# Optimization experiments

Measured on AMD Instinct MI355X. Metric: run time of the kernel, lower is better.

Reference implementation:

```python
import jax, jax.numpy as jnp
import numpy as np

HEADS = 4; C = 128; D = C // HEADS; L = 2
TKG_LEN = 24; NU = 2000; NL = 5000; E = 40000
B = 64; S = 128; MAX_USER = 5000; MAX_LOC = 10000


def _seg_softmax(logits, seg, num_seg):
    # per-destination-node softmax over incoming edges, per head. logits: [E, H]
    m = jax.ops.segment_max(logits, seg, num_segments=num_seg)
    e = jnp.exp(logits - m[seg])
    z = jax.ops.segment_sum(e, seg, num_segments=num_seg)
    return e / (z[seg] + 1e-16)


def _hgt_layer(xu, xl, src_ul, dst_ul, src_lu, dst_lu, wu, bu, wl, bl, ra, rm, rp, skip):
    # PyG HGTConv math. wu/wl: [4,C,C] (k,q,v,a), bu/bl: [4,C];
    # ra/rm: [2,H,D,D] per edge type (0: user->loc, 1: loc->user); rp: [2,H]; skip: [2] (user, loc)
    def kqv(x, w, b):
        return [(x @ w[i] + b[i]).reshape(-1, HEADS, D) for i in range(3)]
    ku, qu, vu = kqv(xu, wu, bu)
    kl, ql, vl = kqv(xl, wl, bl)
    scale = 1.0 / np.sqrt(D).astype(np.float32)

    def edge_msg(k_src, v_src, q_dst, src, dst, a_rel, m_rel, p_rel, n_dst):
        kr = jnp.einsum('nhd,hde->nhe', k_src, a_rel)   # relation-transformed keys
        mr = jnp.einsum('nhd,hde->nhe', v_src, m_rel)   # relation-transformed messages
        logits = (q_dst[dst] * kr[src]).sum(-1) * p_rel * scale  # [E, H]
        alpha = _seg_softmax(logits, dst, n_dst)
        return jax.ops.segment_sum(mr[src] * alpha[..., None], dst, num_segments=n_dst)  # [N,H,D]

    agg_l = edge_msg(ku, vu, ql, src_ul, dst_ul, ra[0], rm[0], rp[0], xl.shape[0])
    agg_u = edge_msg(kl, vl, qu, src_lu, dst_lu, ra[1], rm[1], rp[1], xu.shape[0])

    def update(agg, x, wa, ba, s):
        out = jax.nn.gelu(agg.reshape(-1, C), approximate=False) @ wa + ba
        g = jax.nn.sigmoid(s)
        return g * out + (1.0 - g) * x

    return (update(agg_u, xu, wu[3], bu[3], skip[0]),
            update(agg_l, xl, wl[3], bl[3], skip[1]))


def setup_inputs():
    key = jax.random.key(0)
    ks = jax.random.split(key, 20)
    w = lambda k, shape, s=0.05: jax.random.normal(k, shape, jnp.float32) * s
    user_emb = w(ks[0], (MAX_USER, C), 0.1).at[0].set(0.0)  # padding_idx=0
    loc_emb = w(ks[1], (MAX_LOC, C), 0.1).at[0].set(0.0)
    return dict(
        user_emb=user_emb, loc_emb=loc_emb,
        lin_user_w=w(ks[2], (C, C)), lin_user_b=jnp.zeros((C,), jnp.float32),
        lin_loc_w=w(ks[3], (C, C)), lin_loc_b=jnp.zeros((C,), jnp.float32),
        w_user=w(ks[4], (L, 4, C, C)), b_user=jnp.zeros((L, 4, C), jnp.float32),
        w_loc=w(ks[5], (L, 4, C, C)), b_loc=jnp.zeros((L, 4, C), jnp.float32),
        rel_a=w(ks[6], (L, 2, HEADS, D, D), 1.0 / np.sqrt(D)),
        rel_m=w(ks[7], (L, 2, HEADS, D, D), 1.0 / np.sqrt(D)),
        rel_p=jnp.ones((L, 2, HEADS), jnp.float32),
        skip=jnp.ones((L, 2), jnp.float32),
        lin2_w=w(ks[8], (C, C)), lin2_b=jnp.zeros((C,), jnp.float32),
        user_ids=jax.random.randint(ks[9], (TKG_LEN, NU), 0, MAX_USER),
        loc_ids=jax.random.randint(ks[10], (TKG_LEN, NL), 0, MAX_LOC),
        ei_ul_src=jax.random.randint(ks[11], (TKG_LEN, E), 0, NU),
        ei_ul_dst=jax.random.randint(ks[12], (TKG_LEN, E), 0, NL),
        ei_lu_src=jax.random.randint(ks[13], (TKG_LEN, E), 0, NL),
        ei_lu_dst=jax.random.randint(ks[14], (TKG_LEN, E), 0, NU),
        traj=jax.random.randint(ks[15], (B, S), 0, NL),
        tkg_idx=jax.random.randint(ks[16], (B, S), 0, TKG_LEN),
    )


def reference(user_emb, loc_emb, lin_user_w, lin_user_b, lin_loc_w, lin_loc_b,
              w_user, b_user, w_loc, b_loc, rel_a, rel_m, rel_p, skip,
              lin2_w, lin2_b, user_ids, loc_ids, ei_ul_src, ei_ul_dst,
              ei_lu_src, ei_lu_dst, traj, tkg_idx):
    def encode(uid, lid, sul, dul, slu, dlu):
        # EmbeddingLayer lookup + AggregationLayer: per-node-type Linear + relu, HGT convs, lin2 on locations
        xu = jax.nn.relu(user_emb[uid] @ lin_user_w + lin_user_b)
        xl = jax.nn.relu(loc_emb[lid] @ lin_loc_w + lin_loc_b)
        for i in range(L):
            xu, xl = _hgt_layer(xu, xl, sul, dul, slu, dlu,
                                w_user[i], b_user[i], w_loc[i], b_loc[i],
                                rel_a[i], rel_m[i], rel_p[i], skip[i])
        return xl @ lin2_w + lin2_b

    # the torch loop over tkg_dl snapshots -> vmap over the tkg_len axis
    tkg_out = jax.vmap(encode)(user_ids, loc_ids, ei_ul_src, ei_ul_dst, ei_lu_src, ei_lu_dst)
    # tkg_filter: one-hot mask multiply-sum == direct gather tkg_out[tkg_idx[b,s], traj[b,s]]
    tkg_traj = tkg_out[tkg_idx, traj]  # [B, S, C]
    return (tkg_traj, tkg_out)
```

## Files before the change

### kernel.cpp

```cpp
#include <hip/hip_runtime.h>
#include <math.h>

#define T_LEN 24
#define NUU 2000
#define NLL 5000
#define NE 40000
#define CH 128
#define NH 4
#define HD 32
#define TCHUNK 8

typedef __attribute__((ext_vector_type(8))) short short8;
typedef __attribute__((ext_vector_type(4))) float f32x4;

static inline int cdiv(int a, int b) { return (a + b - 1) / b; }

__device__ __forceinline__ unsigned short f2bf(float x) {
    unsigned u = __float_as_uint(x);
    unsigned r = (u + 0x7fff + ((u >> 16) & 1)) >> 16;
    return (unsigned short)r;
}
__device__ __forceinline__ float bf2f(unsigned short h) {
    return __uint_as_float(((unsigned)h) << 16);
}
__device__ __forceinline__ float2 bf2x(unsigned u) {
    float2 r;
    r.x = __uint_as_float(u << 16);
    r.y = __uint_as_float(u & 0xffff0000u);
    return r;
}

__global__ void fill_zero_int(int* __restrict__ p, int n) {
    int i = blockIdx.x * blockDim.x + threadIdx.x;
    if (i < n) p[i] = 0;
}

__global__ void histo_kernel(const int* __restrict__ dst, int* __restrict__ deg, int n) {
    int idx = blockIdx.x * blockDim.x + threadIdx.x;
    if (idx >= T_LEN * NE) return;
    int t = idx / NE;
    atomicAdd(&deg[t * n + dst[idx]], 1);
}

__global__ __launch_bounds__(256) void scan_off(const int* __restrict__ deg, int* __restrict__ offo,
                                                int* __restrict__ cur, int n) {
    __shared__ int part[256];
    int t = blockIdx.x, tid = threadIdx.x;
    int items = (n + 255) / 256;
    int start = tid * items, end = min(start + items, n);
    const int* dt = deg + t * n;
    int s = 0;
    for (int i = start; i < end; ++i) s += dt[i];
    part[tid] = s;
    __syncthreads();
    for (int d = 1; d < 256; d <<= 1) {
        int v = (tid >= d) ? part[tid - d] : 0;
        __syncthreads();
        part[tid] += v;
        __syncthreads();
    }
    int run = part[tid] - s;
    int* ot = offo + t * (n + 1);
    int* ct = cur + t * n;
    if (tid == 0) ot[0] = 0;
    for (int i = start; i < end; ++i) {
        ct[i] = run;
        run += dt[i];
        ot[i + 1] = run;
    }
}

__global__ void scatter_src(const int* __restrict__ dst, const int* __restrict__ src,
                            int* __restrict__ cur, int* __restrict__ ssrc, int n) {
    int idx = blockIdx.x * blockDim.x + threadIdx.x;
    if (idx >= T_LEN * NE) return;
    int t = idx / NE;
    int d = dst[idx];
    int pos = atomicAdd(&cur[t * n + d], 1);
    ssrc[(size_t)t * NE + pos] = src[idx];
}

__global__ __launch_bounds__(256) void build_fused(
    const float* __restrict__ w, const float* __restrict__ b,
    const float* __restrict__ ra, const float* __restrict__ rm,
    float* __restrict__ Wf, float* __restrict__ bf) {
    int idx = blockIdx.x * 256 + threadIdx.x;
    if (idx >= 128 * 384) return;
    int c = idx / 384, col = idx - c * 384;
    if (col < 128) {
        Wf[c * 384 + col] = w[16384 + c * 128 + col];
        if (c == 0) bf[col] = b[128 + col];
    } else {
        int sec = (col - 128) >> 7;
        int hc = (col - 128) & 127;
        int h = hc >> 5, e2 = hc & 31;
        const float* A = (sec == 0 ? ra : rm) + h * 1024;
        const float* wsrc = w + (sec == 0 ? 0 : 2) * 16384;
        const float* bsrc = b + (sec == 0 ? 0 : 2) * 128;
        float s = 0.f, sb = 0.f;
#pragma unroll
        for (int d = 0; d < 32; ++d) {
            float a = A[d * 32 + e2];
            s += wsrc[c * 128 + h * 32 + d] * a;
            sb += bsrc[h * 32 + d] * a;
        }
        Wf[c * 384 + col] = s;
        if (c == 0) bf[col] = sb;
    }
}

__global__ void bprep_kernel(const float* __restrict__ W, unsigned short* __restrict__ prep, int N) {
    int idx = blockIdx.x * blockDim.x + threadIdx.x;
    if (idx >= 128 * N) return;
    int k = idx / N, n = idx - k * N;
    float v = W[idx];
    unsigned short hi = f2bf(v);
    unsigned short lo = f2bf(v - bf2f(hi));
    int nt = n >> 6, nl = n & 63;
    size_t base = (size_t)nt * 16384 + (size_t)nl * 128 + k;
    prep[base] = hi;
    prep[base + 8192] = lo;
}

template <bool GATHER, int EPI>
__global__ __launch_bounds__(256) void gemm_mfma(
    const float* __restrict__ A, const int* __restrict__ ids,
    const unsigned short* __restrict__ prep, const float* __restrict__ bias,
    float* __restrict__ C, const float* __restrict__ Xold,
    const float* __restrict__ skipPtr, unsigned short* __restrict__ km,
    int M, int NC) {
    __shared__ __align__(16) char smem[65536];

    const int tid = threadIdx.x;
    const int lane = tid & 63;
    const int wid_w = tid >> 6;
    const int wm = wid_w >> 1, wn = wid_w & 1;
    const int l15 = lane & 15, l4 = lane >> 4;

    const int nx = gridDim.x, ny = gridDim.y;
    int flat = blockIdx.y * nx + blockIdx.x;
    int nwg = nx * ny;
    int q = nwg >> 3, r = nwg & 7;
    int xcd = flat & 7, rank = flat >> 3;
    int wgid = (xcd < r ? xcd * (q + 1) : r * (q + 1) + (xcd - r) * q) + rank;
    const int m0 = (wgid / ny) * 128;
    const int n0 = (wgid % ny) * 64;

    const unsigned short* bp = prep + (size_t)(wgid % ny) * 16384;
    short8 bh[2][4], bl[2][4];
#pragma unroll
    for (int nf = 0; nf < 2; ++nf) {
        int ncol = wn * 32 + nf * 16 + l15;
#pragma unroll
        for (int ks = 0; ks < 4; ++ks) {
            size_t off = (size_t)ncol * 128 + ks * 32 + l4 * 8;
            bh[nf][ks] = *(const short8*)(bp + off);
            bl[nf][ks] = *(const short8*)(bp + 8192 + off);
        }
    }

#pragma unroll
    for (int i = 0; i < 16; ++i) {
        int flat2 = i * 256 + tid;
        int rr = flat2 >> 5, c4 = flat2 & 31;
        int gr = m0 + rr;
        if (gr >= M) gr = M - 1;
        int arow = GATHER ? ids[gr] : gr;
        float4 v = *(const float4*)(A + (size_t)arow * 128 + c4 * 4);
        unsigned short h0 = f2bf(v.x), h1 = f2bf(v.y), h2 = f2bf(v.z), h3 = f2bf(v.w);
        unsigned short q0 = f2bf(v.x - bf2f(h0)), q1 = f2bf(v.y - bf2f(h1));
        unsigned short q2 = f2bf(v.z - bf2f(h2)), q3 = f2bf(v.w - bf2f(h3));
        uint2 hp, lp;
        hp.x = (unsigned)h0 | ((unsigned)h1 << 16);
        hp.y = (unsigned)h2 | ((unsigned)h3 << 16);
        lp.x = (unsigned)q0 | ((unsigned)q1 << 16);
        lp.y = (unsigned)q2 | ((unsigned)q3 << 16);
        int off = rr * 256 + ((c4 * 8) ^ ((rr & 7) << 4));
        *(uint2*)(smem + off) = hp;
        *(uint2*)(smem + 32768 + off) = lp;
    }
    __syncthreads();

    f32x4 acc[4][2];
#pragma unroll
    for (int m = 0; m < 4; ++m)
#pragma unroll
        for (int nf = 0; nf < 2; ++nf) acc[m][nf] = (f32x4)0.f;

#pragma unroll
    for (int ks = 0; ks < 4; ++ks) {
        short8 ah[4], al[4];
#pragma unroll
        for (int m = 0; m < 4; ++m) {
            int row = wm * 64 + m * 16 + l15;
            int off = row * 256 + ((ks * 64 + l4 * 16) ^ ((row & 7) << 4));
            ah[m] = *(const short8*)(smem + off);
            al[m] = *(const short8*)(smem + 32768 + off);
        }
#pragma unroll
        for (int m = 0; m < 4; ++m)
#pragma unroll
            for (int nf = 0; nf < 2; ++nf) {
                acc[m][nf] = __builtin_amdgcn_mfma_f32_16x16x32_bf16(al[m], bh[nf][ks], acc[m][nf], 0, 0, 0);
                acc[m][nf] = __builtin_amdgcn_mfma_f32_16x16x32_bf16(ah[m], bl[nf][ks], acc[m][nf], 0, 0, 0);
                acc[m][nf] = __builtin_amdgcn_mfma_f32_16x16x32_bf16(ah[m], bh[nf][ks], acc[m][nf], 0, 0, 0);
            }
    }

    float g = 0.f;
    if (EPI == 2) g = 1.f / (1.f + expf(-skipPtr[0]));
    float bias_v[2];
#pragma unroll
    for (int nf = 0; nf < 2; ++nf) bias_v[nf] = bias[n0 + wn * 32 + nf * 16 + l15];

#pragma unroll
    for (int m = 0; m < 4; ++m) {
#pragma unroll
        for (int nf = 0; nf < 2; ++nf) {
            int gc = n0 + wn * 32 + nf * 16 + l15;
#pragma unroll
            for (int i = 0; i < 4; ++i) {
                int gr = m0 + wm * 64 + m * 16 + l4 * 4 + i;
                if (gr >= M) continue;
                float x = acc[m][nf][i] + bias_v[nf];
                if (EPI == 1) x = fmaxf(x, 0.f);
                if (EPI == 2) {
                    float xo = Xold[(size_t)gr * NC + gc];
                    x = g * x + (1.f - g) * xo;
                }
                if (EPI == 3) {
                    if (gc < 128) C[(size_t)gr * 128 + gc] = x;
                    else km[(size_t)gr * 256 + (gc - 128)] = f2bf(x);
                } else {
                    C[(size_t)gr * NC + gc] = x;
                }
            }
        }
    }
}

__global__ __launch_bounds__(256) void agg_edges(
    const float* __restrict__ qD,
    const unsigned short* __restrict__ kmS,
    const int* __restrict__ off,
    const int* __restrict__ ssrc,
    const float* __restrict__ relp,
    float* __restrict__ agg,
    int nDst, int nSrc, int tBase) {
    int idx = blockIdx.x * 256 + threadIdx.x;
    int total = TCHUNK * nDst * NH * 8;
    if (idx >= total) return;
    int h = idx & 3;
    int slot = (idx >> 2) & 7;
    int node = (idx >> 5) % nDst;
    int tl = (idx >> 5) / nDst;
    int t = tBase + tl;

    size_t drow = (size_t)(tl * nDst + node);
    float p = relp[h] * 0.17677669529663687f;

    const float4* qp = (const float4*)(qD + drow * 128 + h * HD);
    float qr[HD];
#pragma unroll
    for (int j = 0; j < 8; j++) {
        float4 v = qp[j];
        qr[4 * j + 0] = v.x * p; qr[4 * j + 1] = v.y * p;
        qr[4 * j + 2] = v.z * p; qr[4 * j + 3] = v.w * p;
    }

    float m = -INFINITY, z = 0.f;
    float acc[HD];
#pragma unroll
    for (int d = 0; d < HD; d++) acc[d] = 0.f;

    int e0 = off[t * (nDst + 1) + node], e1 = off[t * (nDst + 1) + node + 1];
    const int* ssT = ssrc + (size_t)t * NE;

    for (int i = e0 + slot; i < e1; i += 8) {
        int s = ssT[i];
        const uint4* kp = (const uint4*)(kmS + ((size_t)(tl * nSrc + s)) * 256);
        uint ku[16], mu_[16];
        *(uint4*)(ku + 0) = kp[h * 4 + 0];
        *(uint4*)(ku + 4) = kp[h * 4 + 1];
        *(uint4*)(ku + 8) = kp[h * 4 + 2];
        *(uint4*)(ku + 12) = kp[h * 4 + 3];
        *(uint4*)(mu_ + 0) = kp[16 + h * 4 + 0];
        *(uint4*)(mu_ + 4) = kp[16 + h * 4 + 1];
        *(uint4*)(mu_ + 8) = kp[16 + h * 4 + 2];
        *(uint4*)(mu_ + 12) = kp[16 + h * 4 + 3];

        float dot = 0.f;
#pragma unroll
        for (int j = 0; j < 16; ++j) {
            float2 f = bf2x(ku[j]);
            dot = fmaf(qr[2 * j], f.x, dot);
            dot = fmaf(qr[2 * j + 1], f.y, dot);
        }
        float mn = fmaxf(m, dot);
        float c = __expf(m - mn);
        float w = __expf(dot - mn);
        z = z * c + w;
#pragma unroll
        for (int j = 0; j < 16; ++j) {
            float2 f = bf2x(mu_[j]);
            acc[2 * j] = fmaf(w, f.x, acc[2 * j] * c);
            acc[2 * j + 1] = fmaf(w, f.y, acc[2 * j + 1] * c);
        }
        m = mn;
    }

#pragma unroll
    for (int lm = 4; lm <= 16; lm <<= 1) {
        float mo = __shfl_xor(m, lm);
        float zo = __shfl_xor(z, lm);
        float mn = fmaxf(m, mo);
        float s1 = (m > -INFINITY) ? __expf(m - mn) : 0.f;
        float s2 = (mo > -INFINITY) ? __expf(mo - mn) : 0.f;
        z = z * s1 + zo * s2;
#pragma unroll
        for (int d = 0; d < HD; d++) {
            float ao = __shfl_xor(acc[d], lm);
            acc[d] = acc[d] * s1 + ao * s2;
        }
        m = mn;
    }

    if (slot == 0) {
        float inv = 1.f / (z + 1e-16f);
        float* op = agg + drow * CH + h * HD;
#pragma unroll
        for (int d = 0; d < HD; d++) {
            float v = acc[d] * inv;
            v = 0.5f * v * (1.f + erff(v * 0.70710678118654752f));
            op[d] = v;
        }
    }
}

__global__ void gather_traj(const float* __restrict__ tkg, const int* __restrict__ traj,
                            const int* __restrict__ tki, float* __restrict__ outp) {
    int idx = blockIdx.x * blockDim.x + threadIdx.x;
    if (idx >= 64 * 128 * 128) return;
    int r = idx >> 7, c2 = idx & 127;
    int t = tki[r], n = traj[r];
    outp[idx] = tkg[((size_t)t * NLL + n) * CH + c2];
}

extern "C" void kernel_launch(void* const* d_in, const int* in_sizes, int n_in,
                              void* d_out, int out_size, void* d_ws, size_t ws_size,
                              hipStream_t stream) {
    (void)in_sizes; (void)n_in; (void)out_size; (void)ws_size;
    const float* user_emb = (const float*)d_in[0];
    const float* loc_emb = (const float*)d_in[1];
    const float* lin_user_w = (const float*)d_in[2];
    const float* lin_user_b = (const float*)d_in[3];
    const float* lin_loc_w = (const float*)d_in[4];
    const float* lin_loc_b = (const float*)d_in[5];
    const float* w_user = (const float*)d_in[6];
    const float* b_user = (const float*)d_in[7];
    const float* w_loc = (const float*)d_in[8];
    const float* b_loc = (const float*)d_in[9];
    const float* rel_a = (const float*)d_in[10];
    const float* rel_m = (const float*)d_in[11];
    const float* rel_p = (const float*)d_in[12];
    const float* skip = (const float*)d_in[13];
    const float* lin2_w = (const float*)d_in[14];
    const float* lin2_b = (const float*)d_in[15];
    const int* user_ids = (const int*)d_in[16];
    const int* loc_ids = (const int*)d_in[17];
    const int* ei_ul_src = (const int*)d_in[18];
    const int* ei_ul_dst = (const int*)d_in[19];
    const int* ei_lu_src = (const int*)d_in[20];
    const int* ei_lu_dst = (const int*)d_in[21];
    const int* traj = (const int*)d_in[22];
    const int* tkg_idx = (const int*)d_in[23];
    float* outp = (float*)d_out;

    size_t woff = 0;
    char* base = (char*)d_ws;
    auto carve = [&](size_t bytes) -> void* {
        void* p = base + woff;
        woff += (bytes + 255) & ~(size_t)255;
        return p;
    };
    float* xu = (float*)carve((size_t)T_LEN * NUU * 128 * 4);
    float* xl = (float*)carve((size_t)T_LEN * NLL * 128 * 4);
    float* q_u = (float*)carve((size_t)TCHUNK * NUU * 128 * 4);
    float* q_l = (float*)carve((size_t)TCHUNK * NLL * 128 * 4);
    unsigned short* km_u = (unsigned short*)carve((size_t)TCHUNK * NUU * 256 * 2);
    unsigned short* km_l = (unsigned short*)carve((size_t)TCHUNK * NLL * 256 * 2);
    float* agg_u = (float*)carve((size_t)TCHUNK * NUU * 128 * 4);
    float* agg_l = (float*)carve((size_t)TCHUNK * NLL * 128 * 4);
    float* wf_u = (float*)carve(128 * 384 * 4);
    float* bf_u = (float*)carve(384 * 4);
    float* wf_l = (float*)carve(128 * 384 * 4);
    float* bf_l = (float*)carve(384 * 4);
    int* deg_ul = (int*)carve((size_t)T_LEN * NLL * 4);
    int* cur_ul = (int*)carve((size_t)T_LEN * NLL * 4);
    int* off_ul = (int*)carve((size_t)T_LEN * (NLL + 1) * 4);
    int* ss_ul = (int*)carve((size_t)T_LEN * NE * 4);
    int* deg_lu = (int*)carve((size_t)T_LEN * NUU * 4);
    int* cur_lu = (int*)carve((size_t)T_LEN * NUU * 4);
    int* off_lu = (int*)carve((size_t)T_LEN * (NUU + 1) * 4);
    int* ss_lu = (int*)carve((size_t)T_LEN * NE * 4);
    unsigned short* bp_lin_u = (unsigned short*)carve(128 * 512);
    unsigned short* bp_lin_l = (unsigned short*)carve(128 * 512);
    unsigned short* bp_lin2 = (unsigned short*)carve(128 * 512);
    unsigned short* bp_upd_u[2] = {(unsigned short*)carve(128 * 512), (unsigned short*)carve(128 * 512)};
    unsigned short* bp_upd_l[2] = {(unsigned short*)carve(128 * 512), (unsigned short*)carve(128 * 512)};
    unsigned short* bp_wf_u = (unsigned short*)carve(384 * 512);
    unsigned short* bp_wf_l = (unsigned short*)carve(384 * 512);

    fill_zero_int<<<cdiv(T_LEN * NLL, 256), 256, 0, stream>>>(deg_ul, T_LEN * NLL);
    fill_zero_int<<<cdiv(T_LEN * NUU, 256), 256, 0, stream>>>(deg_lu, T_LEN * NUU);
    histo_kernel<<<cdiv(T_LEN * NE, 256), 256, 0, stream>>>(ei_ul_dst, deg_ul, NLL);
    histo_kernel<<<cdiv(T_LEN * NE, 256), 256, 0, stream>>>(ei_lu_dst, deg_lu, NUU);
    scan_off<<<T_LEN, 256, 0, stream>>>(deg_ul, off_ul, cur_ul, NLL);
    scan_off<<<T_LEN, 256, 0, stream>>>(deg_lu, off_lu, cur_lu, NUU);
    scatter_src<<<cdiv(T_LEN * NE, 256), 256, 0, stream>>>(ei_ul_dst, ei_ul_src, cur_ul, ss_ul, NLL);
    scatter_src<<<cdiv(T_LEN * NE, 256), 256, 0, stream>>>(ei_lu_dst, ei_lu_src, cur_lu, ss_lu, NUU);

    bprep_kernel<<<64, 256, 0, stream>>>(lin_user_w, bp_lin_u, 128);
    bprep_kernel<<<64, 256, 0, stream>>>(lin_loc_w, bp_lin_l, 128);
    bprep_kernel<<<64, 256, 0, stream>>>(lin2_w, bp_lin2, 128);
    for (int l = 0; l < 2; ++l) {
        bprep_kernel<<<64, 256, 0, stream>>>(w_user + (size_t)(l * 4 + 3) * 16384, bp_upd_u[l], 128);
        bprep_kernel<<<64, 256, 0, stream>>>(w_loc + (size_t)(l * 4 + 3) * 16384, bp_upd_l[l], 128);
    }

    gemm_mfma<true, 1><<<dim3(cdiv(T_LEN * NUU, 128), 2), 256, 0, stream>>>(
        user_emb, user_ids, bp_lin_u, lin_user_b, xu, nullptr, nullptr, nullptr, T_LEN * NUU, 128);
    gemm_mfma<true, 1><<<dim3(cdiv(T_LEN * NLL, 128), 2), 256, 0, stream>>>(
        loc_emb, loc_ids, bp_lin_l, lin_loc_b, xl, nullptr, nullptr, nullptr, T_LEN * NLL, 128);

    for (int l = 0; l < 2; ++l) {
        build_fused<<<cdiv(128 * 384, 256), 256, 0, stream>>>(
            w_user + (size_t)l * 4 * 16384, b_user + l * 512,
            rel_a + (size_t)(l * 2 + 0) * 4096, rel_m + (size_t)(l * 2 + 0) * 4096, wf_u, bf_u);
        build_fused<<<cdiv(128 * 384, 256), 256, 0, stream>>>(
            w_loc + (size_t)l * 4 * 16384, b_loc + l * 512,
            rel_a + (size_t)(l * 2 + 1) * 4096, rel_m + (size_t)(l * 2 + 1) * 4096, wf_l, bf_l);
        bprep_kernel<<<192, 256, 0, stream>>>(wf_u, bp_wf_u, 384);
        bprep_kernel<<<192, 256, 0, stream>>>(wf_l, bp_wf_l, 384);

        for (int tb = 0; tb < T_LEN; tb += TCHUNK) {
            const int MU = TCHUNK * NUU;
            const int ML = TCHUNK * NLL;
            float* xu_c = xu + (size_t)tb * NUU * 128;
            float* xl_c = xl + (size_t)tb * NLL * 128;

            gemm_mfma<false, 3><<<dim3(cdiv(MU, 128), 6), 256, 0, stream>>>(
                xu_c, nullptr, bp_wf_u, bf_u, q_u, nullptr, nullptr, km_u, MU, 384);
            gemm_mfma<false, 3><<<dim3(cdiv(ML, 128), 6), 256, 0, stream>>>(
                xl_c, nullptr, bp_wf_l, bf_l, q_l, nullptr, nullptr, km_l, ML, 384);

            agg_edges<<<cdiv(TCHUNK * NLL * NH * 8, 256), 256, 0, stream>>>(
                q_l, km_u, off_ul, ss_ul, rel_p + (l * 2 + 0) * 4, agg_l, NLL, NUU, tb);
            agg_edges<<<cdiv(TCHUNK * NUU * NH * 8, 256), 256, 0, stream>>>(
                q_u, km_l, off_lu, ss_lu, rel_p + (l * 2 + 1) * 4, agg_u, NUU, NLL, tb);

            gemm_mfma<false, 2><<<dim3(cdiv(MU, 128), 2), 256, 0, stream>>>(
                agg_u, nullptr, bp_upd_u[l], b_user + l * 512 + 384,
                xu_c, xu_c, skip + l * 2 + 0, nullptr, MU, 128);
            gemm_mfma<false, 2><<<dim3(cdiv(ML, 128), 2), 256, 0, stream>>>(
                agg_l, nullptr, bp_upd_l[l], b_loc + l * 512 + 384,
                xl_c, xl_c, skip + l * 2 + 1, nullptr, ML, 128);
        }
    }

    float* tkg_out = outp + (size_t)64 * 128 * 128;
    gemm_mfma<false, 0><<<dim3(cdiv(T_LEN * NLL, 128), 2), 256, 0, stream>>>(
        xl, nullptr, bp_lin2, lin2_b, tkg_out, nullptr, nullptr, nullptr, T_LEN * NLL, 128);

    gather_traj<<<cdiv(64 * 128 * 128, 256), 256, 0, stream>>>(tkg_out, traj, tkg_idx, outp);
}
```

Before: 1.659 ms.

## Merge edge-aggregation launches and halve per-node slots with two-edge unrolling

The two per-relation edge attention/aggregation kernels become a single launch that dispatches on block index. Each destination node/head now uses 4 lanes instead of 8. Each lane processes two edges per iteration, issuing both edges' key/message loads together and folding them into a single online-softmax update. This cuts the number of shuffle-reduction steps and launch overhead and raises memory-level parallelism per thread. The costs are higher register pressure and fewer threads in flight. Low-degree nodes may also be less balanced across lanes.

Result: faster. 1.546 ms (-6.8%).

```diff
diff --git a/kernel.cpp b/kernel.cpp
--- a/kernel.cpp
+++ b/kernel.cpp
@@ -239,21 +239,15 @@
     }
 }
 
-__global__ __launch_bounds__(256) void agg_edges(
-    const float* __restrict__ qD,
-    const unsigned short* __restrict__ kmS,
-    const int* __restrict__ off,
-    const int* __restrict__ ssrc,
-    const float* __restrict__ relp,
-    float* __restrict__ agg,
+__device__ __forceinline__ void agg_core(
+    int idx, const float* __restrict__ qD, const unsigned short* __restrict__ kmS,
+    const int* __restrict__ off, const int* __restrict__ ssrc,
+    const float* __restrict__ relp, float* __restrict__ agg,
     int nDst, int nSrc, int tBase) {
-    int idx = blockIdx.x * 256 + threadIdx.x;
-    int total = TCHUNK * nDst * NH * 8;
-    if (idx >= total) return;
     int h = idx & 3;
-    int slot = (idx >> 2) & 7;
-    int node = (idx >> 5) % nDst;
-    int tl = (idx >> 5) / nDst;
+    int slot = (idx >> 2) & 3;
+    int node = (idx >> 4) % nDst;
+    int tl = (idx >> 4) / nDst;
     int t = tBase + tl;
 
     size_t drow = (size_t)(tl * nDst + node);
@@ -276,7 +270,47 @@
     int e0 = off[t * (nDst + 1) + node], e1 = off[t * (nDst + 1) + node + 1];
     const int* ssT = ssrc + (size_t)t * NE;
 
-    for (int i = e0 + slot; i < e1; i += 8) {
+    int i = e0 + slot;
+    for (; i + 4 < e1; i += 8) {
+        int s0 = ssT[i], s1 = ssT[i + 4];
+        const uint4* kp0 = (const uint4*)(kmS + ((size_t)(tl * nSrc + s0)) * 256);
+        const uint4* kp1 = (const uint4*)(kmS + ((size_t)(tl * nSrc + s1)) * 256);
+        uint4 k0a = kp0[h * 4 + 0], k0b = kp0[h * 4 + 1], k0c = kp0[h * 4 + 2], k0d = kp0[h * 4 + 3];
+        uint4 m0a = kp0[16 + h * 4 + 0], m0b = kp0[16 + h * 4 + 1], m0c = kp0[16 + h * 4 + 2], m0d = kp0[16 + h * 4 + 3];
+        uint4 k1a = kp1[h * 4 + 0], k1b = kp1[h * 4 + 1], k1c = kp1[h * 4 + 2], k1d = kp1[h * 4 + 3];
+        uint4 m1a = kp1[16 + h * 4 + 0], m1b = kp1[16 + h * 4 + 1], m1c = kp1[16 + h * 4 + 2], m1d = kp1[16 + h * 4 + 3];
+
+        uint ku0[16], ku1[16], mu0[16], mu1[16];
+        *(uint4*)(ku0 + 0) = k0a; *(uint4*)(ku0 + 4) = k0b; *(uint4*)(ku0 + 8) = k0c; *(uint4*)(ku0 + 12) = k0d;
+        *(uint4*)(mu0 + 0) = m0a; *(uint4*)(mu0 + 4) = m0b; *(uint4*)(mu0 + 8) = m0c; *(uint4*)(mu0 + 12) = m0d;
+        *(uint4*)(ku1 + 0) = k1a; *(uint4*)(ku1 + 4) = k1b; *(uint4*)(ku1 + 8) = k1c; *(uint4*)(ku1 + 12) = k1d;
+        *(uint4*)(mu1 + 0) = m1a; *(uint4*)(mu1 + 4) = m1b; *(uint4*)(mu1 + 8) = m1c; *(uint4*)(mu1 + 12) = m1d;
+
+        float dot0 = 0.f, dot1 = 0.f;
+#pragma unroll
+        for (int j = 0; j < 16; ++j) {
+            float2 f0 = bf2x(ku0[j]);
+            float2 f1 = bf2x(ku1[j]);
+            dot0 = fmaf(qr[2 * j], f0.x, dot0);
+            dot0 = fmaf(qr[2 * j + 1], f0.y, dot0);
+            dot1 = fmaf(qr[2 * j], f1.x, dot1);
+            dot1 = fmaf(qr[2 * j + 1], f1.y, dot1);
+        }
+        float mn = fmaxf(m, fmaxf(dot0, dot1));
+        float c = __expf(m - mn);
+        float w0 = __expf(dot0 - mn);
+        float w1 = __expf(dot1 - mn);
+        z = z * c + w0 + w1;
+#pragma unroll
+        for (int j = 0; j < 16; ++j) {
+            float2 f0 = bf2x(mu0[j]);
+            float2 f1 = bf2x(mu1[j]);
+            acc[2 * j] = fmaf(w1, f1.x, fmaf(w0, f0.x, acc[2 * j] * c));
+            acc[2 * j + 1] = fmaf(w1, f1.y, fmaf(w0, f0.y, acc[2 * j + 1] * c));
+        }
+        m = mn;
+    }
+    if (i < e1) {
         int s = ssT[i];
         const uint4* kp = (const uint4*)(kmS + ((size_t)(tl * nSrc + s)) * 256);
         uint ku[16], mu_[16];
@@ -288,7 +322,6 @@
         *(uint4*)(mu_ + 4) = kp[16 + h * 4 + 1];
         *(uint4*)(mu_ + 8) = kp[16 + h * 4 + 2];
         *(uint4*)(mu_ + 12) = kp[16 + h * 4 + 3];
-
         float dot = 0.f;
 #pragma unroll
         for (int j = 0; j < 16; ++j) {
@@ -310,7 +343,7 @@
     }
 
 #pragma unroll
-    for (int lm = 4; lm <= 16; lm <<= 1) {
+    for (int lm = 4; lm <= 8; lm <<= 1) {
         float mo = __shfl_xor(m, lm);
         float zo = __shfl_xor(z, lm);
         float mn = fmaxf(m, mo);
@@ -334,6 +367,25 @@
             v = 0.5f * v * (1.f + erff(v * 0.70710678118654752f));
             op[d] = v;
         }
+    }
+}
+
+#define UL_B ((TCHUNK * NLL * NH * 4) / 256)
+#define LU_B ((TCHUNK * NUU * NH * 4) / 256)
+__global__ __launch_bounds__(256) void agg_dual(
+    const float* __restrict__ q_l, const unsigned short* __restrict__ km_u,
+    const int* __restrict__ off_ul, const int* __restrict__ ss_ul,
+    const float* __restrict__ relp_ul, float* __restrict__ agg_l,
+    const float* __restrict__ q_u, const unsigned short* __restrict__ km_l,
+    const int* __restrict__ off_lu, const int* __restrict__ ss_lu,
+    const float* __restrict__ relp_lu, float* __restrict__ agg_u,
+    int tBase) {
+    if (blockIdx.x < UL_B) {
+        int idx = blockIdx.x * 256 + threadIdx.x;
+        agg_core(idx, q_l, km_u, off_ul, ss_ul, relp_ul, agg_l, NLL, NUU, tBase);
+    } else {
+        int idx = (blockIdx.x - UL_B) * 256 + threadIdx.x;
+        agg_core(idx, q_u, km_l, off_lu, ss_lu, relp_lu, agg_u, NUU, NLL, tBase);
     }
 }
 
@@ -454,10 +506,9 @@
             gemm_mfma<false, 3><<<dim3(cdiv(ML, 128), 6), 256, 0, stream>>>(
                 xl_c, nullptr, bp_wf_l, bf_l, q_l, nullptr, nullptr, km_l, ML, 384);
 
-            agg_edges<<<cdiv(TCHUNK * NLL * NH * 8, 256), 256, 0, stream>>>(
-                q_l, km_u, off_ul, ss_ul, rel_p + (l * 2 + 0) * 4, agg_l, NLL, NUU, tb);
-            agg_edges<<<cdiv(TCHUNK * NUU * NH * 8, 256), 256, 0, stream>>>(
-                q_u, km_l, off_lu, ss_lu, rel_p + (l * 2 + 1) * 4, agg_u, NUU, NLL, tb);
+            agg_dual<<<UL_B + LU_B, 256, 0, stream>>>(
+                q_l, km_u, off_ul, ss_ul, rel_p + (l * 2 + 0) * 4, agg_l,
+                q_u, km_l, off_lu, ss_lu, rel_p + (l * 2 + 1) * 4, agg_u, tb);
 
             gemm_mfma<false, 2><<<dim3(cdiv(MU, 128), 2), 256, 0, stream>>>(
                 agg_u, nullptr, bp_upd_u[l], b_user + l * 512 + 384,
```
